# Performance work log

Measured on AMD Instinct MI355X. Metric: run time of the kernel, lower is better.

The kernel has to match this reference:

```python
import jax, jax.numpy as jnp
import numpy as np

B, L, D, H, F = 2, 1024, 1024, 16, 4096
DH = D // H
EPS = 1e-6


def _layernorm(x, g, b, eps=1e-5):
    m = jnp.mean(x, axis=-1, keepdims=True)
    v = jnp.mean((x - m) ** 2, axis=-1, keepdims=True)
    return (x - m) / jnp.sqrt(v + eps) * g + b


def setup_inputs() -> dict:
    key = jax.random.key(0)
    ks = jax.random.split(key, 12)

    def w(k, shape):
        return jax.random.normal(k, shape, dtype=jnp.float32) * 0.02

    return {
        "inputs": jax.random.normal(ks[0], (B, L, D), dtype=jnp.float32),
        "attn_mask": jnp.zeros((L, L), dtype=jnp.bool_),
        "Wq": w(ks[1], (D, D)), "bq": jnp.zeros((D,), jnp.float32),
        "Wk": w(ks[2], (D, D)), "bk": jnp.zeros((D,), jnp.float32),
        "Wv": w(ks[3], (D, D)), "bv": jnp.zeros((D,), jnp.float32),
        "Wo": w(ks[4], (D, D)), "bo": jnp.zeros((D,), jnp.float32),
        "ln1_g": jnp.ones((D,), jnp.float32), "ln1_b": jnp.zeros((D,), jnp.float32),
        "W1": w(ks[5], (D, F)), "b1": jnp.zeros((F,), jnp.float32),
        "W2": w(ks[6], (F, D)), "b2": jnp.zeros((D,), jnp.float32),
        "ln2_g": jnp.ones((D,), jnp.float32), "ln2_b": jnp.zeros((D,), jnp.float32),
    }


def _decoder_layer(inputs, Wq, bq, Wk, bk, Wv, bv, Wo, bo,
                   ln1_g, ln1_b, W1, b1, W2, b2, ln2_g, ln2_b):
    Bn, Ln, Dn = inputs.shape

    def heads(W, b):
        # [B,L,D] -> [B,H,L,Dh]
        return (inputs @ W + b).reshape(Bn, Ln, H, DH).transpose(0, 2, 1, 3)

    q = jax.nn.sigmoid(heads(Wq, bq))  # kernel feature map
    k = jax.nn.sigmoid(heads(Wk, bk))
    v = heads(Wv, bv)

    normal = (jnp.arange(Ln, dtype=jnp.float32) + 1.0)[None, None, :]  # [1,1,L]

    sink_in = normal / jnp.einsum('bhld,bhld->bhl', q + EPS, jnp.cumsum(k, axis=2) + EPS)
    src_out = normal / jnp.einsum('bhld,bhld->bhl', k + EPS, jnp.cumsum(q, axis=2) + EPS)

    cons_sink = jnp.einsum('bhld,bhld->bhl', q + EPS,
                           jnp.cumsum(k * src_out[..., None], axis=2) + EPS) / normal
    cons_src = jnp.einsum('bhld,bhld->bhl', k + EPS,
                          jnp.cumsum(q * sink_in[..., None], axis=2) + EPS) / normal
    cons_src = jnp.clip(cons_src, -1.0, 1.0)

    sink_alloc = jax.nn.sigmoid(cons_sink)
    cons_src = jnp.exp(cons_src)
    src_comp = cons_src / jnp.cumsum(cons_src, axis=-1) * normal

    # causal linear attention: cumsum of outer products k v^T, contracted with q
    qs = q * (sink_in / normal)[..., None]           # [B,H,L,Dh]
    vs = v * src_comp[..., None]                     # [B,H,L,Dh]
    kv = jnp.cumsum(jnp.einsum('bhld,bhlm->bhldm', k, vs), axis=2)  # [B,H,L,Dh,Dh]
    x = jnp.einsum('bhld,bhldm->bhlm', qs, kv) * sink_alloc[..., None]

    x = x.transpose(0, 2, 1, 3).reshape(Bn, Ln, Dn)
    attn = x @ Wo + bo

    h = _layernorm(inputs + attn, ln1_g, ln1_b)
    ffn = jax.nn.gelu(h @ W1 + b1, approximate=False) @ W2 + b2
    return _layernorm(h + ffn, ln2_g, ln2_b)


def reference(inputs, attn_mask, Wq, bq, Wk, bk, Wv, bv, Wo, bo,
              ln1_g, ln1_b, W1, b1, W2, b2, ln2_g, ln2_b):
    # attn_mask is unused by the original module (causality comes from cumsum)
    return _decoder_layer(inputs, Wq, bq, Wk, bk, Wv, bv, Wo, bo,
                          ln1_g, ln1_b, W1, b1, W2, b2, ln2_g, ln2_b)
```

## Files before the change

### kernel.cpp

```cpp
#include <hip/hip_runtime.h>
#include <hip/hip_bf16.h>

#define EPS 1e-6f
#define NBH 32
#define LSEQ 1024
#define DHD 64

typedef unsigned short u16;
typedef __bf16 bf16x8 __attribute__((ext_vector_type(8)));
typedef float f32x4 __attribute__((ext_vector_type(4)));

__device__ inline u16 f2bf(float f){
  union { float f; unsigned u; } un; un.f = f;
  unsigned u = un.u;
  u += 0x7fffu + ((u >> 16) & 1u);
  return (u16)(u >> 16);
}

__device__ inline float bf2f(u16 v){
  union { unsigned u; float f; } un; un.u = ((unsigned)v) << 16; return un.f;
}

__device__ inline float wred64(float v){
#pragma unroll
  for (int off = 32; off > 0; off >>= 1) v += __shfl_xor(v, off, 64);
  return v;
}

__device__ inline float wscan64(float v, int lane){
  float run = v;
#pragma unroll
  for (int off = 1; off < 64; off <<= 1){
    float t = __shfl_up(run, off, 64);
    if (lane >= off) run += t;
  }
  return run;
}

__device__ inline float fast_sigmoid(float x){
  return 1.f / (1.f + __expf(-x));
}

__device__ inline void gload_lds16(const u16* g, u16* l){
  __builtin_amdgcn_global_load_lds(
      (const __attribute__((address_space(1))) unsigned int*)g,
      (__attribute__((address_space(3))) unsigned int*)l, 16, 0, 0);
}

__device__ inline void tr_tile2(const float* in, u16* out, int R, int C, int r0, int c0){
  __shared__ float tile[32][33];
  int x = threadIdx.x & 31, y = threadIdx.x >> 5;
#pragma unroll
  for (int j = 0; j < 4; j++)
    tile[y + j*8][x] = in[(size_t)(r0 + y + j*8) * C + c0 + x];
  __syncthreads();
#pragma unroll
  for (int j = 0; j < 4; j++)
    out[(size_t)(c0 + y + j*8) * R + r0 + x] = f2bf(tile[x][y + j*8]);
}

__global__ __launch_bounds__(256) void prep_all(
    const float* __restrict__ inputs, u16* __restrict__ Xbf,
    const float* __restrict__ Wq, const float* __restrict__ Wk,
    const float* __restrict__ Wv, const float* __restrict__ Wo,
    u16* __restrict__ dqkv, u16* __restrict__ dwo,
    const float* __restrict__ W1, const float* __restrict__ W2,
    u16* __restrict__ d1, u16* __restrict__ d2,
    const float* __restrict__ bq, const float* __restrict__ bk,
    const float* __restrict__ bv, float* __restrict__ bqkv,
    float* __restrict__ ckq_zero)
{
  int b = blockIdx.x;
  if (b < 2048){
    int i = b * 256 + threadIdx.x;
    float4 v = reinterpret_cast<const float4*>(inputs)[i];
    ushort4 o; o.x = f2bf(v.x); o.y = f2bf(v.y); o.z = f2bf(v.z); o.w = f2bf(v.w);
    reinterpret_cast<ushort4*>(Xbf)[i] = o;
  } else if (b < 6144){
    int t = b - 2048;
    int z = t >> 10, rem = t & 1023;
    int bx = rem & 31, by = rem >> 5;
    const float* in = (z == 0) ? Wq : (z == 1) ? Wk : (z == 2) ? Wv : Wo;
    u16* out = (z < 3) ? (dqkv + (size_t)z * 1024 * 1024) : dwo;
    tr_tile2(in, out, 1024, 1024, by * 32, bx * 32);
  } else if (b < 14336){
    int t = b - 6144;
    int z = t >> 12, rem = t & 4095;
    int bx = rem & 127, by = rem >> 7;
    if (z == 0) tr_tile2(W1, d1, 1024, 4096, by * 32, bx * 32);
    else        tr_tile2(W2, d2, 4096, 1024, bx * 32, by * 32);
  } else if (b < 14348){
    int i = (b - 14336) * 256 + threadIdx.x;
    if (i < 3072){
      float v = (i < 1024) ? bq[i] : (i < 2048) ? bk[i - 1024] : bv[i - 2048];
      bqkv[i] = v;
    }
  } else {
    int i = (b - 14348) * 256 + threadIdx.x;
    reinterpret_cast<float4*>(ckq_zero)[i] = make_float4(0.f, 0.f, 0.f, 0.f);
  }
}

template<int BM, int BN, int ACT, int OM>
__global__ __launch_bounds__(256) void gemm_mfma(
    const u16* __restrict__ A, const u16* __restrict__ Bt,
    const float* __restrict__ bias, const float* __restrict__ resid,
    float* __restrict__ outF, u16* __restrict__ outB,
    float* __restrict__ cqA, float* __restrict__ ckA,
    int M, int N, int K)
{
  constexpr int BK = 64;
  constexpr int MI = BM / 32;
  constexpr int NJ = BN / 32;
  constexpr int RA = BM / 32;
  constexpr int RB = BN / 32;
  constexpr int NS = RA + RB;
  __shared__ u16 As[2][BM * BK];
  __shared__ u16 Bs[2][BN * BK];
  const int tid = threadIdx.x;
  const int lane = tid & 63, wave = tid >> 6;
  const int lrow = lane & 15, lg = lane >> 4;
  const int m0 = blockIdx.x * BM, n0 = blockIdx.y * BN;
  const int wm = (wave >> 1) * (BM / 2), wn = (wave & 1) * (BN / 2);

  const int ksz = K / gridDim.z;
  const int k_begin = blockIdx.z * ksz;
  const int k_end = k_begin + ksz;

  f32x4 acc[MI][NJ];
#pragma unroll
  for (int i = 0; i < MI; i++)
#pragma unroll
    for (int j = 0; j < NJ; j++) acc[i][j] = (f32x4){0.f, 0.f, 0.f, 0.f};

  const u16* Ab = A + (size_t)m0 * K;
  const u16* Bb = Bt + (size_t)n0 * K;

  const int s0 = ((0 * 4 + lg) ^ (lrow & 7)) * 8;
  const int s1 = ((1 * 4 + lg) ^ (lrow & 7)) * 8;

  auto STAGE = [&](int buf, int k0){
#pragma unroll
    for (int r = 0; r < RA; ++r){
      int c = r * 256 + tid;
      int row = c >> 3;
      int kk = ((c ^ row) & 7) << 3;
      gload_lds16(Ab + (size_t)row * K + k0 + kk, &As[buf][(r * 256 + wave * 64) * 8]);
    }
#pragma unroll
    for (int r = 0; r < RB; ++r){
      int c = r * 256 + tid;
      int row = c >> 3;
      int kk = ((c ^ row) & 7) << 3;
      gload_lds16(Bb + (size_t)row * K + k0 + kk, &Bs[buf][(r * 256 + wave * 64) * 8]);
    }
  };

  STAGE(0, k_begin);
  int cur = 0;
  for (int k0 = k_begin; k0 < k_end; k0 += BK){
    if (k0 + BK < k_end){
      STAGE(cur ^ 1, k0 + BK);
      if constexpr (NS == 8)      asm volatile("s_waitcnt vmcnt(8)" ::: "memory");
      else if constexpr (NS == 6) asm volatile("s_waitcnt vmcnt(6)" ::: "memory");
      else                        asm volatile("s_waitcnt vmcnt(0)" ::: "memory");
    } else {
      asm volatile("s_waitcnt vmcnt(0)" ::: "memory");
    }
    __builtin_amdgcn_s_barrier();
    __builtin_amdgcn_sched_barrier(0);
#pragma unroll
    for (int kh = 0; kh < 2; ++kh){
      const int ss = (kh == 0) ? s0 : s1;
      bf16x8 af[MI], bfv[NJ];
#pragma unroll
      for (int i = 0; i < MI; ++i)
        af[i] = *reinterpret_cast<const bf16x8*>(&As[cur][(wm + i * 16 + lrow) * BK + ss]);
#pragma unroll
      for (int j = 0; j < NJ; ++j)
        bfv[j] = *reinterpret_cast<const bf16x8*>(&Bs[cur][(wn + j * 16 + lrow) * BK + ss]);
#pragma unroll
      for (int i = 0; i < MI; ++i)
#pragma unroll
        for (int j = 0; j < NJ; ++j)
          acc[i][j] = __builtin_amdgcn_mfma_f32_16x16x32_bf16(af[i], bfv[j], acc[i][j], 0, 0, 0);
    }
    __builtin_amdgcn_s_barrier();
    cur ^= 1;
  }

  float csum[NJ];
#pragma unroll
  for (int j = 0; j < NJ; ++j) csum[j] = 0.f;

#pragma unroll
  for (int i = 0; i < MI; ++i){
#pragma unroll
    for (int j = 0; j < NJ; ++j){
      int col = n0 + wn + j * 16 + lrow;
      float bv = (OM < 4 && bias) ? bias[col] : 0.f;
#pragma unroll
      for (int r = 0; r < 4; ++r){
        int row = m0 + wm + i * 16 + lg * 4 + r;
        float x = acc[i][j][r] + bv;
        if (OM == 1){
          if (col < 2048){ x = fast_sigmoid(x); csum[j] += x; }
          int which = col >> 10, cc = col & 1023, h = cc >> 6, d = cc & 63;
          int b = row >> 10, l = row & 1023;
          outB[(size_t)which * (2048ull * 1024) +
               (((size_t)(b * 16 + h)) * 1024 + l) * 64 + d] = f2bf(x);
        } else if (OM == 4){
          outF[((size_t)blockIdx.z * M + row) * N + col] = x;
        } else if (OM == 5){
          outB[((size_t)blockIdx.z * M + row) * N + col] = f2bf(x);
        } else {
          if (ACT == 2){
            float u = 0.7978845608f * (x + 0.044715f * x * x * x);
            float e = __expf(2.f * u);
            x = 0.5f * x * (2.f - 2.f / (e + 1.f));
          }
          outB[(size_t)row * N + col] = f2bf(x);
        }
      }
    }
  }
  if (OM == 1){
#pragma unroll
    for (int j = 0; j < NJ; ++j){
      int col = n0 + wn + j * 16 + lrow;
      if (col < 2048){
        int which = col >> 10, cc = col & 1023, h = cc >> 6, d = cc & 63;
        int rowbase = m0 + wm;
        int bh = (rowbase >> 10) * 16 + h;
        int chunk = (rowbase & 1023) >> 6;
        float* dst = (which == 0) ? cqA : ckA;
        atomicAdd(&dst[((size_t)bh * 16 + chunk) * 64 + d], csum[j]);
      }
    }
  }
}

__global__ __launch_bounds__(256) void sink_tile(
    const u16* __restrict__ q, const u16* __restrict__ k,
    const float* __restrict__ ck, const float* __restrict__ cq,
    float* __restrict__ sink_in, float* __restrict__ src_out,
    float* __restrict__ cso, float* __restrict__ cqsi)
{
  int blk = blockIdx.x, bh = blk >> 4, c = blk & 15;
  int tid = threadIdx.x, lane = tid & 63, wave = tid >> 6;
  __shared__ float qT[64][65], kT[64][65], G[64][66];
  __shared__ float PK[64], PQ[64];
  __shared__ float rk[64], rq[64], crk[64], crq[64], siv[64], sov[64];
  __shared__ float rd[2][4][64];
  size_t base = ((size_t)bh * LSEQ + c * 64) * DHD;
  const u16* qb = q + base; const u16* kb = k + base;
  for (int c4 = tid; c4 < 1024; c4 += 256){
    int l = c4 >> 4, d0 = (c4 & 15) * 4;
    ushort4 qv = *reinterpret_cast<const ushort4*>(qb + c4 * 4);
    qT[d0+0][l] = bf2f(qv.x); qT[d0+1][l] = bf2f(qv.y);
    qT[d0+2][l] = bf2f(qv.z); qT[d0+3][l] = bf2f(qv.w);
    ushort4 kv = *reinterpret_cast<const ushort4*>(kb + c4 * 4);
    kT[d0+0][l] = bf2f(kv.x); kT[d0+1][l] = bf2f(kv.y);
    kT[d0+2][l] = bf2f(kv.z); kT[d0+3][l] = bf2f(kv.w);
  }
  if (tid < 64){
    float pk = 0.f, pq = 0.f;
    for (int cc = 0; cc < c; cc++){
      pk += ck[((size_t)bh * 16 + cc) * 64 + tid];
      pq += cq[((size_t)bh * 16 + cc) * 64 + tid];
    }
    PK[tid] = pk; PQ[tid] = pq;
  }
  __syncthreads();
  float sumPK = wred64(PK[lane]);
  float sumPQ = wred64(PQ[lane]);
  {
    int l = lane, g = wave;
    float qrow[64];
#pragma unroll
    for (int d = 0; d < 64; d++) qrow[d] = qT[d][l];
    float p[16] = {};
    for (int d = 0; d < 64; d++){
      float qv = qrow[d];
#pragma unroll
      for (int j4 = 0; j4 < 4; j4++){
        float4 kk = *reinterpret_cast<const float4*>(&kT[d][g * 16 + j4 * 4]);
        p[j4*4+0] += qv * kk.x; p[j4*4+1] += qv * kk.y;
        p[j4*4+2] += qv * kk.z; p[j4*4+3] += qv * kk.w;
      }
    }
#pragma unroll
    for (int jj = 0; jj < 16; jj++) G[l][g * 16 + jj] = p[jj];
  }
  {
    float pk_ = 0.f, pq_ = 0.f;
#pragma unroll
    for (int d = wave * 16; d < wave * 16 + 16; d++){
      pk_ += kT[d][lane]; pq_ += qT[d][lane];
    }
    rd[0][wave][lane] = pk_; rd[1][wave][lane] = pq_;
  }
  __syncthreads();
  if (tid < 64){
    rk[tid] = rd[0][0][tid] + rd[0][1][tid] + rd[0][2][tid] + rd[0][3][tid];
    rq[tid] = rd[1][0][tid] + rd[1][1][tid] + rd[1][2][tid] + rd[1][3][tid];
  }
  __syncthreads();
  if (wave == 0)      crk[lane] = wscan64(rk[lane], lane);
  else if (wave == 1) crq[lane] = wscan64(rq[lane], lane);
  __syncthreads();
  {
    int l = lane;
    float p1 = 0.f, p2 = 0.f;
#pragma unroll
    for (int j = wave * 16; j < wave * 16 + 16; j++){
      float g1 = (j <= l) ? G[l][j] : 0.f;
      p1 += g1 + qT[j][l] * PK[j];
      float g2 = (j <= l) ? G[j][l] : 0.f;
      p2 += g2 + kT[j][l] * PQ[j];
    }
    rd[0][wave][l] = p1; rd[1][wave][l] = p2;
  }
  __syncthreads();
  const float EPS2 = 64.f * EPS * EPS;
  if (tid < 64){
    int l = tid;
    float s1 = rd[0][0][l] + rd[0][1][l] + rd[0][2][l] + rd[0][3][l];
    float s2 = rd[1][0][l] + rd[1][1][l] + rd[1][2][l] + rd[1][3][l];
    int L = c * 64 + l; float nrm = (float)(L + 1);
    float den1 = s1 + EPS * rq[l] + EPS * (sumPK + crk[l]) + EPS2;
    float den2 = s2 + EPS * rk[l] + EPS * (sumPQ + crq[l]) + EPS2;
    float si_ = nrm / den1, so_ = nrm / den2;
    sink_in[(size_t)bh * LSEQ + L] = si_;
    src_out[(size_t)bh * LSEQ + L] = so_;
    siv[l] = si_; sov[l] = so_;
  }
  __syncthreads();
  float s1 = 0.f, s2 = 0.f;
  for (int l = wave * 16; l < wave * 16 + 16; l++){
    s1 += sov[l] * kT[lane][l];
    s2 += siv[l] * qT[lane][l];
  }
  rd[0][wave][lane] = s1; rd[1][wave][lane] = s2;
  __syncthreads();
  if (wave == 0){
    cso [(size_t)blk * 64 + lane] = rd[0][0][lane] + rd[0][1][lane] + rd[0][2][lane] + rd[0][3][lane];
    cqsi[(size_t)blk * 64 + lane] = rd[1][0][lane] + rd[1][1][lane] + rd[1][2][lane] + rd[1][3][lane];
  }
}

__global__ __launch_bounds__(256) void cons_tile(
    const u16* __restrict__ q, const u16* __restrict__ k,
    const float* __restrict__ cso, const float* __restrict__ cqsi,
    const float* __restrict__ sink_in, const float* __restrict__ src_out,
    float* __restrict__ sa, float* __restrict__ ebuf)
{
  int blk = blockIdx.x, bh = blk >> 4, c = blk & 15;
  int tid = threadIdx.x, lane = tid & 63, wave = tid >> 6;
  __shared__ float qT[64][65], kT[64][65], G[64][66];
  __shared__ float PKso[64], PQsi[64];
  __shared__ float rk[64], rq[64], cwrk[64], cwrq[64], siv[64], sov[64];
  __shared__ float rd[2][4][64];
  size_t base = ((size_t)bh * LSEQ + c * 64) * DHD;
  const u16* qb = q + base; const u16* kb = k + base;
  for (int c4 = tid; c4 < 1024; c4 += 256){
    int l = c4 >> 4, d0 = (c4 & 15) * 4;
    ushort4 qv = *reinterpret_cast<const ushort4*>(qb + c4 * 4);
    qT[d0+0][l] = bf2f(qv.x); qT[d0+1][l] = bf2f(qv.y);
    qT[d0+2][l] = bf2f(qv.z); qT[d0+3][l] = bf2f(qv.w);
    ushort4 kv = *reinterpret_cast<const ushort4*>(kb + c4 * 4);
    kT[d0+0][l] = bf2f(kv.x); kT[d0+1][l] = bf2f(kv.y);
    kT[d0+2][l] = bf2f(kv.z); kT[d0+3][l] = bf2f(kv.w);
  }
  if (tid < 64){
    float pk = 0.f, pq = 0.f;
    for (int cc = 0; cc < c; cc++){
      pk += cso [((size_t)bh * 16 + cc) * 64 + tid];
      pq += cqsi[((size_t)bh * 16 + cc) * 64 + tid];
    }
    PKso[tid] = pk; PQsi[tid] = pq;
  } else if (tid < 128){
    int l = tid - 64;
    sov[l] = src_out[(size_t)bh * LSEQ + c * 64 + l];
    siv[l] = sink_in[(size_t)bh * LSEQ + c * 64 + l];
  }
  __syncthreads();
  float sumPKso = wred64(PKso[lane]);
  float sumPQsi = wred64(PQsi[lane]);
  {
    int l = lane, g = wave;
    float qrow[64];
#pragma unroll
    for (int d = 0; d < 64; d++) qrow[d] = qT[d][l];
    float p[16] = {};
    for (int d = 0; d < 64; d++){
      float qv = qrow[d];
#pragma unroll
      for (int j4 = 0; j4 < 4; j4++){
        float4 kk = *reinterpret_cast<const float4*>(&kT[d][g * 16 + j4 * 4]);
        p[j4*4+0] += qv * kk.x; p[j4*4+1] += qv * kk.y;
        p[j4*4+2] += qv * kk.z; p[j4*4+3] += qv * kk.w;
      }
    }
#pragma unroll
    for (int jj = 0; jj < 16; jj++) G[l][g * 16 + jj] = p[jj];
  }
  {
    float pk_ = 0.f, pq_ = 0.f;
#pragma unroll
    for (int d = wave * 16; d < wave * 16 + 16; d++){
      pk_ += kT[d][lane]; pq_ += qT[d][lane];
    }
    rd[0][wave][lane] = pk_; rd[1][wave][lane] = pq_;
  }
  __syncthreads();
  if (tid < 64){
    rk[tid] = rd[0][0][tid] + rd[0][1][tid] + rd[0][2][tid] + rd[0][3][tid];
    rq[tid] = rd[1][0][tid] + rd[1][1][tid] + rd[1][2][tid] + rd[1][3][tid];
  }
  __syncthreads();
  if (wave == 0)      cwrk[lane] = wscan64(sov[lane] * rk[lane], lane);
  else if (wave == 1) cwrq[lane] = wscan64(siv[lane] * rq[lane], lane);
  __syncthreads();
  {
    int l = lane;
    float p3 = 0.f, p4 = 0.f;
#pragma unroll
    for (int j = wave * 16; j < wave * 16 + 16; j++){
      float g3 = (j <= l) ? sov[j] * G[l][j] : 0.f;
      p3 += g3 + qT[j][l] * PKso[j];
      float g4 = (j <= l) ? siv[j] * G[j][l] : 0.f;
      p4 += g4 + kT[j][l] * PQsi[j];
    }
    rd[0][wave][l] = p3; rd[1][wave][l] = p4;
  }
  __syncthreads();
  const float EPS2 = 64.f * EPS * EPS;
  if (tid < 64){
    int l = tid;
    float s3 = rd[0][0][l] + rd[0][1][l] + rd[0][2][l] + rd[0][3][l];
    float s4 = rd[1][0][l] + rd[1][1][l] + rd[1][2][l] + rd[1][3][l];
    int L = c * 64 + l; float nrm = (float)(L + 1);
    float cs = (s3 + EPS * rq[l] + EPS * (sumPKso + cwrk[l]) + EPS2) / nrm;
    sa[(size_t)bh * LSEQ + L] = fast_sigmoid(cs);
    float c2 = (s4 + EPS * rk[l] + EPS * (sumPQsi + cwrq[l]) + EPS2) / nrm;
    c2 = fminf(1.f, fmaxf(-1.f, c2));
    ebuf[(size_t)bh * LSEQ + L] = __expf(c2);
  }
}

__global__ __launch_bounds__(64) void srccomp_kernel(const float* __restrict__ ebuf, float* __restrict__ sc){
  int bh = blockIdx.x; int lane = threadIdx.x;
  const float* eb = ebuf + (size_t)bh * LSEQ;
  float loc[16]; float s = 0.f;
#pragma unroll
  for (int i = 0; i < 16; i++){ loc[i] = eb[lane * 16 + i]; s += loc[i]; }
  float run = wscan64(s, lane);
  float acc = run - s;
  float* scb = sc + (size_t)bh * LSEQ;
#pragma unroll
  for (int i = 0; i < 16; i++){
    acc += loc[i];
    scb[lane * 16 + i] = loc[i] / acc * (float)(lane * 16 + i + 1);
  }
}

__global__ __launch_bounds__(256) void phaseA(const u16* __restrict__ k, const u16* __restrict__ v,
                                              const float* __restrict__ sc, u16* __restrict__ S){
  int blk = blockIdx.x; int bh = blk >> 4, c = blk & 15;
  __shared__ float ks[64][68], vss[64][68];
  __shared__ float vc[64];
  int tid = threadIdx.x;
  size_t base = ((size_t)bh * LSEQ + c * 64) * DHD;
  const u16* kb = k + base; const u16* vb = v + base;
  if (tid < 64) vc[tid] = sc[(size_t)bh * LSEQ + c * 64 + tid];
  __syncthreads();
  for (int c4 = tid; c4 < 1024; c4 += 256){
    int l = c4 >> 4, d0 = (c4 & 15) * 4;
    ushort4 kv = *reinterpret_cast<const ushort4*>(kb + c4 * 4);
    ks[l][d0+0] = bf2f(kv.x); ks[l][d0+1] = bf2f(kv.y);
    ks[l][d0+2] = bf2f(kv.z); ks[l][d0+3] = bf2f(kv.w);
    ushort4 vv = *reinterpret_cast<const ushort4*>(vb + c4 * 4);
    float w = vc[l];
    vss[l][d0+0] = bf2f(vv.x) * w; vss[l][d0+1] = bf2f(vv.y) * w;
    vss[l][d0+2] = bf2f(vv.z) * w; vss[l][d0+3] = bf2f(vv.w) * w;
  }
  __syncthreads();
  if (c == 15) return;
  int m = tid >> 2, dg = tid & 3;
  float acc[16] = {};
  for (int l = 0; l < 64; l++){
    float vm = vss[l][m];
#pragma unroll
    for (int d4 = 0; d4 < 4; d4++){
      float4 kk = *reinterpret_cast<const float4*>(&ks[l][dg * 16 + d4 * 4]);
      acc[d4*4+0] += vm * kk.x; acc[d4*4+1] += vm * kk.y;
      acc[d4*4+2] += vm * kk.z; acc[d4*4+3] += vm * kk.w;
    }
  }
  u16* Sb = S + (size_t)blk * 4096 + m * 64 + dg * 16;
#pragma unroll
  for (int d4 = 0; d4 < 4; d4++){
    ushort4 o;
    o.x = f2bf(acc[d4*4+0]); o.y = f2bf(acc[d4*4+1]);
    o.z = f2bf(acc[d4*4+2]); o.w = f2bf(acc[d4*4+3]);
    *reinterpret_cast<ushort4*>(Sb + d4 * 4) = o;
  }
}

__global__ __launch_bounds__(256) void phaseC(const u16* __restrict__ q, const u16* __restrict__ k,
                                              const u16* __restrict__ v, const u16* __restrict__ S,
                                              const float* __restrict__ sink_in, const float* __restrict__ sc,
                                              const float* __restrict__ sa, u16* __restrict__ x){
  int blk = blockIdx.x; int bh = blk >> 4, c = blk & 15;
  int b = bh >> 4, h = bh & 15;
  __shared__ float qp[64][66];
  __shared__ float kT[64][68];
  __shared__ float vss[64][68];
  __shared__ float kvs[64][68];
  __shared__ float qc[64], vc[64];
  int tid = threadIdx.x;
  size_t base = ((size_t)bh * LSEQ + c * 64) * DHD;
  const u16* qb = q + base; const u16* kb = k + base; const u16* vb = v + base;
  if (tid < 64){
    int L = c * 64 + tid;
    qc[tid] = sink_in[(size_t)bh * LSEQ + L] / (float)(L + 1);
    vc[tid] = sc[(size_t)bh * LSEQ + L];
  }
  {
    int off16 = tid * 16;
    float accp[16] = {};
    for (int cc = 0; cc < c; cc++){
      size_t idx = ((size_t)bh * 16 + cc) * 4096 + off16;
#pragma unroll
      for (int t4 = 0; t4 < 4; t4++){
        ushort4 sv = *reinterpret_cast<const ushort4*>(S + idx + t4 * 4);
        accp[t4*4+0] += bf2f(sv.x); accp[t4*4+1] += bf2f(sv.y);
        accp[t4*4+2] += bf2f(sv.z); accp[t4*4+3] += bf2f(sv.w);
      }
    }
#pragma unroll
    for (int e = 0; e < 16; e++){
      int j = off16 + e;
      kvs[j >> 6][j & 63] = accp[e];
    }
  }
  __syncthreads();
  for (int c4 = tid; c4 < 1024; c4 += 256){
    int l = c4 >> 4, d0 = (c4 & 15) * 4;
    float qw = qc[l], vw = vc[l];
    ushort4 qv = *reinterpret_cast<const ushort4*>(qb + c4 * 4);
    qp[d0+0][l] = bf2f(qv.x) * qw; qp[d0+1][l] = bf2f(qv.y) * qw;
    qp[d0+2][l] = bf2f(qv.z) * qw; qp[d0+3][l] = bf2f(qv.w) * qw;
    ushort4 kv4 = *reinterpret_cast<const ushort4*>(kb + c4 * 4);
    kT[d0+0][l] = bf2f(kv4.x); kT[d0+1][l] = bf2f(kv4.y);
    kT[d0+2][l] = bf2f(kv4.z); kT[d0+3][l] = bf2f(kv4.w);
    ushort4 vv = *reinterpret_cast<const ushort4*>(vb + c4 * 4);
    vss[l][d0+0] = bf2f(vv.x) * vw; vss[l][d0+1] = bf2f(vv.y) * vw;
    vss[l][d0+2] = bf2f(vv.z) * vw; vss[l][d0+3] = bf2f(vv.w) * vw;
  }
  __syncthreads();
  int l = tid & 63, g = tid >> 6;
  float qrow[64];
#pragma unroll
  for (int d = 0; d < 64; d++) qrow[d] = qp[d][l];
  __syncthreads();

  float p[16] = {};
  for (int d = 0; d < 64; d++){
    float qv = qrow[d];
#pragma unroll
    for (int j4 = 0; j4 < 4; j4++){
      float4 kk = *reinterpret_cast<const float4*>(&kT[d][g * 16 + j4 * 4]);
      p[j4*4+0] += qv * kk.x; p[j4*4+1] += qv * kk.y;
      p[j4*4+2] += qv * kk.z; p[j4*4+3] += qv * kk.w;
    }
  }
#pragma unroll
  for (int jj = 0; jj < 16; jj++){
    int j = g * 16 + jj;
    qp[l][j] = (j <= l) ? p[jj] : 0.f;
  }
  __syncthreads();

  float acc[16];
#pragma unroll
  for (int mm = 0; mm < 16; mm++){
    float a = 0.f;
#pragma unroll
    for (int d4 = 0; d4 < 16; d4++){
      float4 kv4 = *reinterpret_cast<const float4*>(&kvs[g * 16 + mm][d4 * 4]);
      a += qrow[d4*4+0]*kv4.x + qrow[d4*4+1]*kv4.y + qrow[d4*4+2]*kv4.z + qrow[d4*4+3]*kv4.w;
    }
    acc[mm] = a;
  }
  for (int j = 0; j < 64; j++){
    float pv = qp[l][j];
#pragma unroll
    for (int m4 = 0; m4 < 4; m4++){
      float4 vv = *reinterpret_cast<const float4*>(&vss[j][g * 16 + m4 * 4]);
      acc[m4*4+0] += pv * vv.x; acc[m4*4+1] += pv * vv.y;
      acc[m4*4+2] += pv * vv.z; acc[m4*4+3] += pv * vv.w;
    }
  }
  float sav = sa[(size_t)bh * LSEQ + c * 64 + l];
  u16* xo = x + ((size_t)(b * 1024 + c * 64 + l)) * 1024 + h * 64 + g * 16;
#pragma unroll
  for (int mm = 0; mm < 16; mm++) xo[mm] = f2bf(acc[mm] * sav);
}

__global__ __launch_bounds__(256) void ln_fused2b(
    const u16* __restrict__ p0, const u16* __restrict__ p1,
    const float* __restrict__ resid, const float* __restrict__ bias,
    const float* __restrict__ g, const float* __restrict__ b,
    float* __restrict__ out, u16* __restrict__ outbf){
  int row = blockIdx.x; int tid = threadIdx.x;
  int lane = tid & 63, wave = tid >> 6;
  size_t off = (size_t)row * 1024 + tid * 4;
  ushort4 a0 = *reinterpret_cast<const ushort4*>(p0 + off);
  ushort4 a1 = *reinterpret_cast<const ushort4*>(p1 + off);
  float4 rr = *reinterpret_cast<const float4*>(resid + off);
  float4 bb = *reinterpret_cast<const float4*>(bias + tid * 4);
  float4 v = make_float4(bf2f(a0.x) + bf2f(a1.x) + rr.x + bb.x,
                         bf2f(a0.y) + bf2f(a1.y) + rr.y + bb.y,
                         bf2f(a0.z) + bf2f(a1.z) + rr.z + bb.z,
                         bf2f(a0.w) + bf2f(a1.w) + rr.w + bb.w);
  float s = v.x + v.y + v.z + v.w;
  float s2 = v.x*v.x + v.y*v.y + v.z*v.z + v.w*v.w;
  s = wred64(s); s2 = wred64(s2);
  __shared__ float red[2][4];
  if (lane == 0){ red[0][wave] = s; red[1][wave] = s2; }
  __syncthreads();
  float S = red[0][0] + red[0][1] + red[0][2] + red[0][3];
  float S2 = red[1][0] + red[1][1] + red[1][2] + red[1][3];
  float mean = S * (1.f / 1024.f);
  float var = S2 * (1.f / 1024.f) - mean * mean;
  float inv = rsqrtf(var + 1e-5f);
  float4 gv = *reinterpret_cast<const float4*>(g + tid * 4);
  float4 bv = *reinterpret_cast<const float4*>(b + tid * 4);
  float y0 = (v.x - mean) * inv * gv.x + bv.x;
  float y1 = (v.y - mean) * inv * gv.y + bv.y;
  float y2 = (v.z - mean) * inv * gv.z + bv.z;
  float y3 = (v.w - mean) * inv * gv.w + bv.w;
  *reinterpret_cast<float4*>(out + off) = make_float4(y0, y1, y2, y3);
  ushort4 o; o.x = f2bf(y0); o.y = f2bf(y1); o.z = f2bf(y2); o.w = f2bf(y3);
  *reinterpret_cast<ushort4*>(outbf + off) = o;
}

__global__ __launch_bounds__(256) void ln_fused4b(
    const u16* __restrict__ p0, const u16* __restrict__ p1,
    const u16* __restrict__ p2, const u16* __restrict__ p3,
    const float* __restrict__ resid, const float* __restrict__ bias,
    const float* __restrict__ g, const float* __restrict__ b,
    float* __restrict__ out){
  int row = blockIdx.x; int tid = threadIdx.x;
  int lane = tid & 63, wave = tid >> 6;
  size_t off = (size_t)row * 1024 + tid * 4;
  ushort4 u0 = *reinterpret_cast<const ushort4*>(p0 + off);
  ushort4 u1 = *reinterpret_cast<const ushort4*>(p1 + off);
  ushort4 u2 = *reinterpret_cast<const ushort4*>(p2 + off);
  ushort4 u3 = *reinterpret_cast<const ushort4*>(p3 + off);
  float4 rr = *reinterpret_cast<const float4*>(resid + off);
  float4 bb = *reinterpret_cast<const float4*>(bias + tid * 4);
  float4 v = make_float4(
      bf2f(u0.x) + bf2f(u1.x) + bf2f(u2.x) + bf2f(u3.x) + rr.x + bb.x,
      bf2f(u0.y) + bf2f(u1.y) + bf2f(u2.y) + bf2f(u3.y) + rr.y + bb.y,
      bf2f(u0.z) + bf2f(u1.z) + bf2f(u2.z) + bf2f(u3.z) + rr.z + bb.z,
      bf2f(u0.w) + bf2f(u1.w) + bf2f(u2.w) + bf2f(u3.w) + rr.w + bb.w);
  float s = v.x + v.y + v.z + v.w;
  float s2 = v.x*v.x + v.y*v.y + v.z*v.z + v.w*v.w;
  s = wred64(s); s2 = wred64(s2);
  __shared__ float red[2][4];
  if (lane == 0){ red[0][wave] = s; red[1][wave] = s2; }
  __syncthreads();
  float S = red[0][0] + red[0][1] + red[0][2] + red[0][3];
  float S2 = red[1][0] + red[1][1] + red[1][2] + red[1][3];
  float mean = S * (1.f / 1024.f);
  float var = S2 * (1.f / 1024.f) - mean * mean;
  float inv = rsqrtf(var + 1e-5f);
  float4 gv = *reinterpret_cast<const float4*>(g + tid * 4);
  float4 bv = *reinterpret_cast<const float4*>(b + tid * 4);
  float y0 = (v.x - mean) * inv * gv.x + bv.x;
  float y1 = (v.y - mean) * inv * gv.y + bv.y;
  float y2 = (v.z - mean) * inv * gv.z + bv.z;
  float y3 = (v.w - mean) * inv * gv.w + bv.w;
  *reinterpret_cast<float4*>(out + off) = make_float4(y0, y1, y2, y3);
}

extern "C" void kernel_launch(void* const* d_in, const int* in_sizes, int n_in,
                              void* d_out, int out_size, void* d_ws, size_t ws_size,
                              hipStream_t stream){
  (void)in_sizes; (void)n_in; (void)out_size; (void)ws_size;
  const float* inputs = (const float*)d_in[0];
  const float* Wq = (const float*)d_in[2];  const float* bq = (const float*)d_in[3];
  const float* Wk = (const float*)d_in[4];  const float* bk = (const float*)d_in[5];
  const float* Wv = (const float*)d_in[6];  const float* bv = (const float*)d_in[7];
  const float* Wo = (const float*)d_in[8];  const float* bo = (const float*)d_in[9];
  const float* ln1g = (const float*)d_in[10]; const float* ln1b = (const float*)d_in[11];
  const float* W1 = (const float*)d_in[12]; const float* b1 = (const float*)d_in[13];
  const float* W2 = (const float*)d_in[14]; const float* b2 = (const float*)d_in[15];
  const float* ln2g = (const float*)d_in[16]; const float* ln2b = (const float*)d_in[17];
  float* out = (float*)d_out;

  char* wsp = (char*)d_ws; size_t off = 0;
  auto alloc = [&](size_t bytes) -> void* {
    off = (off + 255) & ~(size_t)255;
    void* p = wsp + off; off += bytes; return p;
  };
  const size_t MD = (size_t)2048 * 1024;
  u16* Xbf    = (u16*)alloc(MD * 2);
  u16* WqkvT  = (u16*)alloc((size_t)3 * 1024 * 1024 * 2);
  u16* WoT    = (u16*)alloc((size_t)1024 * 1024 * 2);
  u16* W1T    = (u16*)alloc((size_t)4096 * 1024 * 2);
  u16* W2T    = (u16*)alloc((size_t)4096 * 1024 * 2);
  float* bqkv = (float*)alloc(3072 * 4);
  u16* qkvb   = (u16*)alloc(3 * MD * 2);
  u16* qb = qkvb; u16* kb = qkvb + MD; u16* vb = qkvb + 2 * MD;
  float* quad = (float*)alloc(4 * MD * 4);
  u16* Sbuf   = (u16*)quad;
  float* ckb  = (float*)alloc((size_t)512 * 64 * 4);
  float* cqb  = (float*)alloc((size_t)512 * 64 * 4);
  float* csob = (float*)alloc((size_t)512 * 64 * 4);
  float* cqsib= (float*)alloc((size_t)512 * 64 * 4);
  float* sink_in = (float*)alloc(NBH * LSEQ * 4);
  float* src_out = (float*)alloc(NBH * LSEQ * 4);
  float* sabuf   = (float*)alloc(NBH * LSEQ * 4);
  float* ebuf    = (float*)alloc(NBH * LSEQ * 4);
  float* scbuf   = (float*)alloc(NBH * LSEQ * 4);
  u16* xatt   = (u16*)alloc(MD * 2);
  u16* g1     = (u16*)alloc((size_t)2048 * 4096 * 2);
  float* hbuf  = quad;
  u16* hbf     = (u16*)(quad + MD);
  u16* wopart  = (u16*)(quad + 2 * MD);
  u16* partb   = (u16*)(quad + 2 * MD);

  prep_all<<<14412, 256, 0, stream>>>(inputs, Xbf, Wq, Wk, Wv, Wo, WqkvT, WoT,
                                      W1, W2, W1T, W2T, bq, bk, bv, bqkv, ckb);

  gemm_mfma<128, 64, 0, 1><<<dim3(16, 48), 256, 0, stream>>>(
      Xbf, WqkvT, bqkv, nullptr, nullptr, qkvb, cqb, ckb, 2048, 3072, 1024);

  sink_tile<<<512, 256, 0, stream>>>(qb, kb, ckb, cqb, sink_in, src_out, csob, cqsib);
  cons_tile<<<512, 256, 0, stream>>>(qb, kb, csob, cqsib, sink_in, src_out, sabuf, ebuf);
  srccomp_kernel<<<32, 64, 0, stream>>>(ebuf, scbuf);

  phaseA<<<512, 256, 0, stream>>>(kb, vb, scbuf, Sbuf);
  phaseC<<<512, 256, 0, stream>>>(qb, kb, vb, Sbuf, sink_in, scbuf, sabuf, xatt);

  gemm_mfma<128, 64, 0, 5><<<dim3(16, 16, 2), 256, 0, stream>>>(
      xatt, WoT, nullptr, nullptr, nullptr, wopart, nullptr, nullptr, 2048, 1024, 1024);
  ln_fused2b<<<2048, 256, 0, stream>>>(wopart, wopart + MD, inputs, bo, ln1g, ln1b, hbuf, hbf);

  gemm_mfma<128, 128, 2, 3><<<dim3(16, 32), 256, 0, stream>>>(
      hbf, W1T, b1, nullptr, nullptr, g1, nullptr, nullptr, 2048, 4096, 1024);
  gemm_mfma<128, 128, 0, 5><<<dim3(16, 8, 4), 256, 0, stream>>>(
      g1, W2T, nullptr, nullptr, nullptr, partb, nullptr, nullptr, 2048, 1024, 4096);
  ln_fused4b<<<2048, 256, 0, stream>>>(partb, partb + MD, partb + 2 * MD, partb + 3 * MD,
                                       hbuf, b2, ln2g, ln2b, out);
}
```

Measured before the change: 187.8 us.

## Fold src_comp prefix scan into phaseA/phaseC and prefetch q/k/v into registers

Removes the separate srccomp_kernel launch and its scbuf round trip. phaseA and phaseC now each recompute the per-chunk src_comp weights from ebuf using a wave-level reduction over earlier chunks plus an in-chunk scan. The q/k/v global loads are issued into registers before that computation so they overlap with it. phaseA exits early for the last chunk, and the S prefix accumulation in phaseC uses wider 16-byte loads. The trade-off is redundant scan work per block, whose cost grows with the chunk index.

```diff
diff --git a/kernel.cpp b/kernel.cpp
--- a/kernel.cpp
+++ b/kernel.cpp
@@ -45,6 +45,13 @@
   __builtin_amdgcn_global_load_lds(
       (const __attribute__((address_space(1))) unsigned int*)g,
       (__attribute__((address_space(3))) unsigned int*)l, 16, 0, 0);
+}
+
+__device__ inline void acc8(float* a, uint4 w){
+  a[0] += bf2f((u16)(w.x & 0xffff)); a[1] += bf2f((u16)(w.x >> 16));
+  a[2] += bf2f((u16)(w.y & 0xffff)); a[3] += bf2f((u16)(w.y >> 16));
+  a[4] += bf2f((u16)(w.z & 0xffff)); a[5] += bf2f((u16)(w.z >> 16));
+  a[6] += bf2f((u16)(w.w & 0xffff)); a[7] += bf2f((u16)(w.w >> 16));
 }
 
 __device__ inline void tr_tile2(const float* in, u16* out, int R, int C, int r0, int c0){
@@ -449,44 +456,43 @@
   }
 }
 
-__global__ __launch_bounds__(64) void srccomp_kernel(const float* __restrict__ ebuf, float* __restrict__ sc){
-  int bh = blockIdx.x; int lane = threadIdx.x;
-  const float* eb = ebuf + (size_t)bh * LSEQ;
-  float loc[16]; float s = 0.f;
-#pragma unroll
-  for (int i = 0; i < 16; i++){ loc[i] = eb[lane * 16 + i]; s += loc[i]; }
-  float run = wscan64(s, lane);
-  float acc = run - s;
-  float* scb = sc + (size_t)bh * LSEQ;
-#pragma unroll
-  for (int i = 0; i < 16; i++){
-    acc += loc[i];
-    scb[lane * 16 + i] = loc[i] / acc * (float)(lane * 16 + i + 1);
-  }
-}
-
 __global__ __launch_bounds__(256) void phaseA(const u16* __restrict__ k, const u16* __restrict__ v,
-                                              const float* __restrict__ sc, u16* __restrict__ S){
+                                              const float* __restrict__ ebuf, u16* __restrict__ S){
   int blk = blockIdx.x; int bh = blk >> 4, c = blk & 15;
+  if (c == 15) return;
   __shared__ float ks[64][68], vss[64][68];
   __shared__ float vc[64];
-  int tid = threadIdx.x;
+  int tid = threadIdx.x, lane = tid & 63, wave = tid >> 6;
   size_t base = ((size_t)bh * LSEQ + c * 64) * DHD;
   const u16* kb = k + base; const u16* vb = v + base;
-  if (tid < 64) vc[tid] = sc[(size_t)bh * LSEQ + c * 64 + tid];
-  __syncthreads();
-  for (int c4 = tid; c4 < 1024; c4 += 256){
+  ushort4 kr[4], vr[4];
+#pragma unroll
+  for (int it = 0; it < 4; it++){
+    int c4 = tid + it * 256;
+    kr[it] = *reinterpret_cast<const ushort4*>(kb + c4 * 4);
+    vr[it] = *reinterpret_cast<const ushort4*>(vb + c4 * 4);
+  }
+  if (wave == 0){
+    const float* eb = ebuf + (size_t)bh * LSEQ;
+    float basep = 0.f;
+    for (int cc = 0; cc < c; cc++) basep += eb[cc * 64 + lane];
+    float bsum = wred64(basep);
+    float ev = eb[c * 64 + lane];
+    float cums = bsum + wscan64(ev, lane);
+    vc[lane] = ev / cums * (float)(c * 64 + lane + 1);
+  }
+  __syncthreads();
+#pragma unroll
+  for (int it = 0; it < 4; it++){
+    int c4 = tid + it * 256;
     int l = c4 >> 4, d0 = (c4 & 15) * 4;
-    ushort4 kv = *reinterpret_cast<const ushort4*>(kb + c4 * 4);
-    ks[l][d0+0] = bf2f(kv.x); ks[l][d0+1] = bf2f(kv.y);
-    ks[l][d0+2] = bf2f(kv.z); ks[l][d0+3] = bf2f(kv.w);
-    ushort4 vv = *reinterpret_cast<const ushort4*>(vb + c4 * 4);
+    ks[l][d0+0] = bf2f(kr[it].x); ks[l][d0+1] = bf2f(kr[it].y);
+    ks[l][d0+2] = bf2f(kr[it].z); ks[l][d0+3] = bf2f(kr[it].w);
     float w = vc[l];
-    vss[l][d0+0] = bf2f(vv.x) * w; vss[l][d0+1] = bf2f(vv.y) * w;
-    vss[l][d0+2] = bf2f(vv.z) * w; vss[l][d0+3] = bf2f(vv.w) * w;
-  }
-  __syncthreads();
-  if (c == 15) return;
+    vss[l][d0+0] = bf2f(vr[it].x) * w; vss[l][d0+1] = bf2f(vr[it].y) * w;
+    vss[l][d0+2] = bf2f(vr[it].z) * w; vss[l][d0+3] = bf2f(vr[it].w) * w;
+  }
+  __syncthreads();
   int m = tid >> 2, dg = tid & 3;
   float acc[16] = {};
   for (int l = 0; l < 64; l++){
@@ -510,7 +516,7 @@
 
 __global__ __launch_bounds__(256) void phaseC(const u16* __restrict__ q, const u16* __restrict__ k,
                                               const u16* __restrict__ v, const u16* __restrict__ S,
-                                              const float* __restrict__ sink_in, const float* __restrict__ sc,
+                                              const float* __restrict__ sink_in, const float* __restrict__ ebuf,
                                               const float* __restrict__ sa, u16* __restrict__ x){
   int blk = blockIdx.x; int bh = blk >> 4, c = blk & 15;
   int b = bh >> 4, h = bh & 15;
@@ -519,25 +525,37 @@
   __shared__ float vss[64][68];
   __shared__ float kvs[64][68];
   __shared__ float qc[64], vc[64];
-  int tid = threadIdx.x;
+  int tid = threadIdx.x, lane = tid & 63, wave = tid >> 6;
   size_t base = ((size_t)bh * LSEQ + c * 64) * DHD;
   const u16* qb = q + base; const u16* kb = k + base; const u16* vb = v + base;
-  if (tid < 64){
-    int L = c * 64 + tid;
-    qc[tid] = sink_in[(size_t)bh * LSEQ + L] / (float)(L + 1);
-    vc[tid] = sc[(size_t)bh * LSEQ + L];
+  ushort4 qr[4], kr[4], vr[4];
+#pragma unroll
+  for (int it = 0; it < 4; it++){
+    int c4 = tid + it * 256;
+    qr[it] = *reinterpret_cast<const ushort4*>(qb + c4 * 4);
+    kr[it] = *reinterpret_cast<const ushort4*>(kb + c4 * 4);
+    vr[it] = *reinterpret_cast<const ushort4*>(vb + c4 * 4);
+  }
+  if (wave == 0){
+    int L = c * 64 + lane;
+    qc[lane] = sink_in[(size_t)bh * LSEQ + L] / (float)(L + 1);
+    const float* eb = ebuf + (size_t)bh * LSEQ;
+    float basep = 0.f;
+    for (int cc = 0; cc < c; cc++) basep += eb[cc * 64 + lane];
+    float bsum = wred64(basep);
+    float ev = eb[c * 64 + lane];
+    float cums = bsum + wscan64(ev, lane);
+    vc[lane] = ev / cums * (float)(L + 1);
   }
   {
     int off16 = tid * 16;
     float accp[16] = {};
     for (int cc = 0; cc < c; cc++){
       size_t idx = ((size_t)bh * 16 + cc) * 4096 + off16;
-#pragma unroll
-      for (int t4 = 0; t4 < 4; t4++){
-        ushort4 sv = *reinterpret_cast<const ushort4*>(S + idx + t4 * 4);
-        accp[t4*4+0] += bf2f(sv.x); accp[t4*4+1] += bf2f(sv.y);
-        accp[t4*4+2] += bf2f(sv.z); accp[t4*4+3] += bf2f(sv.w);
-      }
+      const uint4* sp = reinterpret_cast<const uint4*>(S + idx);
+      uint4 w0 = sp[0], w1 = sp[1];
+      acc8(&accp[0], w0);
+      acc8(&accp[8], w1);
     }
 #pragma unroll
     for (int e = 0; e < 16; e++){
@@ -546,18 +564,17 @@
     }
   }
   __syncthreads();
-  for (int c4 = tid; c4 < 1024; c4 += 256){
+#pragma unroll
+  for (int it = 0; it < 4; it++){
+    int c4 = tid + it * 256;
     int l = c4 >> 4, d0 = (c4 & 15) * 4;
     float qw = qc[l], vw = vc[l];
-    ushort4 qv = *reinterpret_cast<const ushort4*>(qb + c4 * 4);
-    qp[d0+0][l] = bf2f(qv.x) * qw; qp[d0+1][l] = bf2f(qv.y) * qw;
-    qp[d0+2][l] = bf2f(qv.z) * qw; qp[d0+3][l] = bf2f(qv.w) * qw;
-    ushort4 kv4 = *reinterpret_cast<const ushort4*>(kb + c4 * 4);
-    kT[d0+0][l] = bf2f(kv4.x); kT[d0+1][l] = bf2f(kv4.y);
-    kT[d0+2][l] = bf2f(kv4.z); kT[d0+3][l] = bf2f(kv4.w);
-    ushort4 vv = *reinterpret_cast<const ushort4*>(vb + c4 * 4);
-    vss[l][d0+0] = bf2f(vv.x) * vw; vss[l][d0+1] = bf2f(vv.y) * vw;
-    vss[l][d0+2] = bf2f(vv.z) * vw; vss[l][d0+3] = bf2f(vv.w) * vw;
+    qp[d0+0][l] = bf2f(qr[it].x) * qw; qp[d0+1][l] = bf2f(qr[it].y) * qw;
+    qp[d0+2][l] = bf2f(qr[it].z) * qw; qp[d0+3][l] = bf2f(qr[it].w) * qw;
+    kT[d0+0][l] = bf2f(kr[it].x); kT[d0+1][l] = bf2f(kr[it].y);
+    kT[d0+2][l] = bf2f(kr[it].z); kT[d0+3][l] = bf2f(kr[it].w);
+    vss[l][d0+0] = bf2f(vr[it].x) * vw; vss[l][d0+1] = bf2f(vr[it].y) * vw;
+    vss[l][d0+2] = bf2f(vr[it].z) * vw; vss[l][d0+3] = bf2f(vr[it].w) * vw;
   }
   __syncthreads();
   int l = tid & 63, g = tid >> 6;
@@ -726,7 +743,6 @@
   float* src_out = (float*)alloc(NBH * LSEQ * 4);
   float* sabuf   = (float*)alloc(NBH * LSEQ * 4);
   float* ebuf    = (float*)alloc(NBH * LSEQ * 4);
-  float* scbuf   = (float*)alloc(NBH * LSEQ * 4);
   u16* xatt   = (u16*)alloc(MD * 2);
   u16* g1     = (u16*)alloc((size_t)2048 * 4096 * 2);
   float* hbuf  = quad;
@@ -742,10 +758,9 @@
 
   sink_tile<<<512, 256, 0, stream>>>(qb, kb, ckb, cqb, sink_in, src_out, csob, cqsib);
   cons_tile<<<512, 256, 0, stream>>>(qb, kb, csob, cqsib, sink_in, src_out, sabuf, ebuf);
-  srccomp_kernel<<<32, 64, 0, stream>>>(ebuf, scbuf);
-
-  phaseA<<<512, 256, 0, stream>>>(kb, vb, scbuf, Sbuf);
-  phaseC<<<512, 256, 0, stream>>>(qb, kb, vb, Sbuf, sink_in, scbuf, sabuf, xatt);
+
+  phaseA<<<512, 256, 0, stream>>>(kb, vb, ebuf, Sbuf);
+  phaseC<<<512, 256, 0, stream>>>(qb, kb, vb, Sbuf, sink_in, ebuf, sabuf, xatt);
 
   gemm_mfma<128, 64, 0, 5><<<dim3(16, 16, 2), 256, 0, stream>>>(
       xatt, WoT, nullptr, nullptr, nullptr, wopart, nullptr, nullptr, 2048, 1024, 1024);
```

Result: slower. 192.8 us (+2.6%).
